# Kernel tuning notes

Hardware: AMD Instinct MI355X
Metric: run time of the kernel (lower is better)

The kernel has to match this reference:

```python
import jax, jax.numpy as jnp
import numpy as np

SL, BS, E, H, PF, STRIDE, SHIFT = 2048, 2, 1024, 16, 16, 1, 0
DH = E // H  # 64


def setup_inputs() -> dict:
    key = jax.random.key(0)
    ks = jax.random.split(key, 6)
    s = 0.02
    return {
        'x': jax.random.normal(ks[0], (SL, BS, E), jnp.float32),
        'ln_g': jnp.ones((E,), jnp.float32),
        'ln_b': jnp.zeros((E,), jnp.float32),
        'Wq': jax.random.normal(ks[1], (E, E), jnp.float32) * s,
        'bq': jnp.zeros((E,), jnp.float32),
        'Wk': jax.random.normal(ks[2], (E, E), jnp.float32) * s,
        'bk': jnp.zeros((E,), jnp.float32),
        'Wv': jax.random.normal(ks[3], (E, E), jnp.float32) * s,
        'bv': jnp.zeros((E,), jnp.float32),
        'Wo': jax.random.normal(ks[4], (E, E), jnp.float32) * s,
        'bo': jnp.zeros((E,), jnp.float32),
    }


def _layernorm(x, g, b, eps=1e-5):
    m = x.mean(-1, keepdims=True)
    v = jnp.var(x, axis=-1, keepdims=True)
    return (x - m) * jax.lax.rsqrt(v + eps) * g + b


def _sparsify(context, h):
    # faithful to sparsify(): r = (arange(h)+1)*stride - pf + shift (+ arange(pf)), mod c
    c = context.shape[0]
    base = (jnp.arange(h) + 1) * STRIDE - PF + SHIFT          # [h]
    idx = (base[None, :] + jnp.arange(PF)[:, None]) % c       # [pf, h]
    return context[idx.reshape(-1)].reshape(PF, h, context.shape[1], context.shape[2])


def reference(x, ln_g, ln_b, Wq, bq, Wk, bk, Wv, bv, Wo, bo):
    sl, bs, e = x.shape
    residual = x
    xn = _layernorm(x, ln_g, ln_b)
    # gather pf-sized local context window per query position (modular wrap)
    fetch = _sparsify(xn, sl)                                  # [pf, sl, bs, E]
    # per-token query (length-1) attending to its pf gathered keys
    q = (xn @ Wq + bq).reshape(sl, bs, H, DH)                  # [sl,bs,H,dh]
    k = (fetch @ Wk + bk).reshape(PF, sl, bs, H, DH)           # [pf,sl,bs,H,dh]
    v = (fetch @ Wv + bv).reshape(PF, sl, bs, H, DH)
    scale = 1.0 / jnp.sqrt(jnp.float32(DH))
    scores = jnp.einsum('sbhd,psbhd->sbhp', q, k) * scale      # [sl,bs,H,pf]
    attn = jax.nn.softmax(scores, axis=-1)
    out = jnp.einsum('sbhp,psbhd->sbhd', attn, v).reshape(sl, bs, e)
    out = out @ Wo + bo                                        # output projection
    # dropout is a no-op in eval
    return residual + out
```

## Files before the change

kernel.cpp:

```cpp
#include <hip/hip_runtime.h>
#include <cstdint>
#include <cstddef>

#define SLEN 2048
#define BSZ  2
#define EDIM 1024
#define NHEAD 16
#define DHEAD 64
#define PFW  16
#define NTOK (SLEN*BSZ)

#define BK 32

typedef __attribute__((ext_vector_type(8))) short short8;
typedef __attribute__((ext_vector_type(4))) float floatx4;

__device__ __forceinline__ short f2bf(float f) {
  union { float f; uint32_t u; } v; v.f = f;
  uint32_t r = v.u + 0x7fffu + ((v.u >> 16) & 1u);
  return (short)(r >> 16);
}
__device__ __forceinline__ float bf2f(short s) {
  union { uint32_t u; float f; } v; v.u = ((uint32_t)(uint16_t)s) << 16;
  return v.f;
}

__device__ __forceinline__ void async16(const void* g, void* l) {
  __builtin_amdgcn_global_load_lds((const __attribute__((address_space(1))) void*)g,
                                   (__attribute__((address_space(3))) void*)l,
                                   16, 0, 0);
}

__global__ __launch_bounds__(256) void prep_kernel(
    const float* __restrict__ x, const float* __restrict__ g,
    const float* __restrict__ b, short* __restrict__ xn,
    const float* __restrict__ W0, const float* __restrict__ W1,
    const float* __restrict__ W2, const float* __restrict__ W3,
    short* __restrict__ Wt_base)
{
  const int bid = blockIdx.x;
  const int tid = threadIdx.x;

  if (bid < NTOK) {
    const int row = bid;
    const float4 v = ((const float4*)(x + (size_t)row * EDIM))[tid];
    float s  = v.x + v.y + v.z + v.w;
    float ss = v.x * v.x + v.y * v.y + v.z * v.z + v.w * v.w;
#pragma unroll
    for (int off = 32; off; off >>= 1) {
      s  += __shfl_xor(s, off);
      ss += __shfl_xor(ss, off);
    }
    __shared__ float ws_s[4], ws_ss[4];
    const int lane = tid & 63, wave = tid >> 6;
    if (lane == 0) { ws_s[wave] = s; ws_ss[wave] = ss; }
    __syncthreads();
    s  = ws_s[0] + ws_s[1] + ws_s[2] + ws_s[3];
    ss = ws_ss[0] + ws_ss[1] + ws_ss[2] + ws_ss[3];

    const float mean = s * (1.0f / EDIM);
    const float var  = ss * (1.0f / EDIM) - mean * mean;
    const float rs   = rsqrtf(var + 1e-5f);

    const float4 gv = ((const float4*)g)[tid];
    const float4 bv = ((const float4*)b)[tid];
    short4 o;
    o.x = f2bf((v.x - mean) * rs * gv.x + bv.x);
    o.y = f2bf((v.y - mean) * rs * gv.y + bv.y);
    o.z = f2bf((v.z - mean) * rs * gv.z + bv.z);
    o.w = f2bf((v.w - mean) * rs * gv.w + bv.w);
    ((short4*)(xn + (size_t)row * EDIM))[tid] = o;
  } else {
    const int t = bid - NTOK;
    const int z = t >> 10;
    const int rem = t & 1023;
    const int n0 = (rem & 31) * 32;
    const int k0 = (rem >> 5) * 32;
    const float* W = (z == 0) ? W0 : (z == 1) ? W1 : (z == 2) ? W2 : W3;
    short* Wt = Wt_base + (size_t)z * EDIM * EDIM;

    __shared__ float tile[32][33];
    const int tx = tid & 31;
    const int ty = tid >> 5;
#pragma unroll
    for (int i = 0; i < 4; ++i)
      tile[ty + i * 8][tx] = W[(size_t)(k0 + ty + i * 8) * EDIM + n0 + tx];
    __syncthreads();
#pragma unroll
    for (int i = 0; i < 4; ++i)
      Wt[(size_t)(n0 + ty + i * 8) * EDIM + k0 + tx] = f2bf(tile[tx][ty + i * 8]);
  }
}

__global__ __launch_bounds__(256) void gemm_qkv(
    const short* __restrict__ xn, const short* __restrict__ Wt_base,
    const float* __restrict__ bq, const float* __restrict__ bk,
    const float* __restrict__ bv, short* __restrict__ qkv_base)
{
  __shared__ short As[128 * BK];
  __shared__ short Bs[128 * BK];

  const int bid  = blockIdx.x;
  const int xcd  = bid & 7;
  const int slot = bid >> 3;
  const int nz   = xcd * 3 + slot / 32;
  const int mt   = slot & 31;
  const int z    = nz >> 3;
  const int nt   = nz & 7;

  const short* Bt   = Wt_base + (size_t)z * EDIM * EDIM;
  const float* bias = (z == 0) ? bq : (z == 1) ? bk : bv;
  short* out        = qkv_base + (size_t)z * NTOK * EDIM;

  const int bm = mt * 128;
  const int bn = nt * 128;
  const int tid  = threadIdx.x;
  const int lane = tid & 63;
  const int wave = tid >> 6;

  floatx4 acc[4][4];
#pragma unroll
  for (int i = 0; i < 4; ++i)
#pragma unroll
    for (int j = 0; j < 4; ++j) { floatx4 zz = {0.f, 0.f, 0.f, 0.f}; acc[i][j] = zz; }

  const int lrow = lane >> 2;
  const int lcol = (lane & 3) * 8;
  const short* gA0 = xn + (size_t)(bm + wave * 32 + lrow) * EDIM + lcol;
  const short* gA1 = gA0 + (size_t)16 * EDIM;
  const short* gB0 = Bt + (size_t)(bn + wave * 32 + lrow) * EDIM + lcol;
  const short* gB1 = gB0 + (size_t)16 * EDIM;
  short* lA0 = As + wave * 1024;
  short* lA1 = lA0 + 512;
  short* lB0 = Bs + wave * 1024;
  short* lB1 = lB0 + 512;

  const int wm = (wave >> 1) * 64;
  const int wn = (wave & 1) * 64;
  const int fr = lane & 15;
  const int fq = (lane >> 4) * 8;

  for (int k0 = 0; k0 < EDIM; k0 += BK) {
    async16(gA0, lA0); async16(gA1, lA1);
    async16(gB0, lB0); async16(gB1, lB1);
    gA0 += BK; gA1 += BK; gB0 += BK; gB1 += BK;
    __syncthreads();

    short8 af[4], bf[4];
#pragma unroll
    for (int mi = 0; mi < 4; ++mi)
      af[mi] = *(const short8*)(As + (size_t)(wm + mi * 16 + fr) * BK + fq);
#pragma unroll
    for (int ni = 0; ni < 4; ++ni)
      bf[ni] = *(const short8*)(Bs + (size_t)(wn + ni * 16 + fr) * BK + fq);
#pragma unroll
    for (int mi = 0; mi < 4; ++mi)
#pragma unroll
      for (int ni = 0; ni < 4; ++ni)
        acc[mi][ni] = __builtin_amdgcn_mfma_f32_16x16x32_bf16(
            af[mi], bf[ni], acc[mi][ni], 0, 0, 0);
    __syncthreads();
  }

  const int r0 = bm + wm + ((lane >> 4) * 4);
  const int c0 = bn + wn + (lane & 15);
#pragma unroll
  for (int mi = 0; mi < 4; ++mi)
#pragma unroll
    for (int ni = 0; ni < 4; ++ni) {
      const floatx4 v = acc[mi][ni];
      const int col = c0 + ni * 16;
      const float bb = bias[col];
#pragma unroll
      for (int r = 0; r < 4; ++r) {
        const int row = r0 + mi * 16 + r;
        out[(size_t)row * EDIM + col] = f2bf(v[r] + bb);
      }
    }
}

__global__ __launch_bounds__(256) void gemm_o(
    const short* __restrict__ Aattn, const short* __restrict__ Wot,
    const float* __restrict__ bo, const float* __restrict__ residual,
    float* __restrict__ out)
{
  __shared__ short As[64 * BK];
  __shared__ short Bs[128 * BK];
  const int bm = blockIdx.x * 64;
  const int bn = blockIdx.y * 128;
  const int tid  = threadIdx.x;
  const int lane = tid & 63;
  const int wave = tid >> 6;

  floatx4 acc[2][4];
#pragma unroll
  for (int i = 0; i < 2; ++i)
#pragma unroll
    for (int j = 0; j < 4; ++j) { floatx4 zz = {0.f, 0.f, 0.f, 0.f}; acc[i][j] = zz; }

  const int lrow = lane >> 2;
  const int lcol = (lane & 3) * 8;
  const short* gA0 = Aattn + (size_t)(bm + wave * 16 + lrow) * EDIM + lcol;
  const short* gB0 = Wot + (size_t)(bn + wave * 32 + lrow) * EDIM + lcol;
  const short* gB1 = gB0 + (size_t)16 * EDIM;
  short* lA0 = As + wave * 512;
  short* lB0 = Bs + wave * 1024;
  short* lB1 = lB0 + 512;

  const int wm = (wave >> 1) * 32;
  const int wn = (wave & 1) * 64;
  const int fr = lane & 15;
  const int fq = (lane >> 4) * 8;

  for (int k0 = 0; k0 < EDIM; k0 += BK) {
    async16(gA0, lA0);
    async16(gB0, lB0); async16(gB1, lB1);
    gA0 += BK; gB0 += BK; gB1 += BK;
    __syncthreads();

    short8 af[2], bf[4];
#pragma unroll
    for (int mi = 0; mi < 2; ++mi)
      af[mi] = *(const short8*)(As + (size_t)(wm + mi * 16 + fr) * BK + fq);
#pragma unroll
    for (int ni = 0; ni < 4; ++ni)
      bf[ni] = *(const short8*)(Bs + (size_t)(wn + ni * 16 + fr) * BK + fq);
#pragma unroll
    for (int mi = 0; mi < 2; ++mi)
#pragma unroll
      for (int ni = 0; ni < 4; ++ni)
        acc[mi][ni] = __builtin_amdgcn_mfma_f32_16x16x32_bf16(
            af[mi], bf[ni], acc[mi][ni], 0, 0, 0);
    __syncthreads();
  }

  const int r0 = bm + wm + ((lane >> 4) * 4);
  const int c0 = bn + wn + (lane & 15);
#pragma unroll
  for (int mi = 0; mi < 2; ++mi)
#pragma unroll
    for (int ni = 0; ni < 4; ++ni) {
      const floatx4 v = acc[mi][ni];
      const int col = c0 + ni * 16;
      const float bb = bo[col];
#pragma unroll
      for (int r = 0; r < 4; ++r) {
        const int row = r0 + mi * 16 + r;
        const size_t idx = (size_t)row * EDIM + col;
        out[idx] = residual[idx] + v[r] + bb;
      }
    }
}

#define VT_LD 80
#define PB_LD 40

__global__ __launch_bounds__(256) void attn_mfma(
    const short* __restrict__ Q, const short* __restrict__ K,
    const short* __restrict__ V, short* __restrict__ O)
{
  const int tid  = threadIdx.x;
  const int lane = tid & 63;
  const int wave = tid >> 6;
  const int quad = lane >> 4;
  const int l16  = lane & 15;

  const int bh = blockIdx.y;
  const int h  = bh & (NHEAD - 1);
  const int b  = bh >> 4;
  const int s_blk = blockIdx.x * 64;
  const int col0  = h * DHEAD;

  __shared__ __align__(16) short VT[64 * VT_LD];
  __shared__ __align__(16) short Pb[4][16 * PB_LD];

  for (int task = tid; task < 320; task += 256) {
    const int kp  = task >> 3;
    const int dg  = task & 7;
    const int kk0 = kp * 2;
    int sA = s_blk - 15 + kk0;
    int sB = sA + 1;
    if (sA < 0) sA += SLEN;  if (sA >= SLEN) sA -= SLEN;
    if (sB < 0) sB += SLEN;  if (sB >= SLEN) sB -= SLEN;
    const short8 vA = *(const short8*)(V + (size_t)(sA * BSZ + b) * EDIM + col0 + dg * 8);
    const short8 vB = *(const short8*)(V + (size_t)(sB * BSZ + b) * EDIM + col0 + dg * 8);
#pragma unroll
    for (int j = 0; j < 8; ++j) {
      const int d = dg * 8 + j;
      const uint32_t pack = (uint32_t)(uint16_t)vA[j] | ((uint32_t)(uint16_t)vB[j] << 16);
      *(uint32_t*)&VT[d * VT_LD + kk0] = pack;
    }
  }

  const int sw = s_blk + wave * 16;
  short8 aq[2];
  {
    const size_t base = (size_t)((sw + l16) * BSZ + b) * EDIM + col0 + quad * 8;
    aq[0] = *(const short8*)(Q + base);
    aq[1] = *(const short8*)(Q + base + 32);
  }
  short8 bkf[2][2];
#pragma unroll
  for (int T = 0; T < 2; ++T) {
    int ks = sw - 15 + T * 16 + l16;
    if (ks < 0) ks += SLEN;
    if (ks >= SLEN) ks -= SLEN;
    const size_t base = (size_t)(ks * BSZ + b) * EDIM + col0 + quad * 8;
    bkf[T][0] = *(const short8*)(K + base);
    bkf[T][1] = *(const short8*)(K + base + 32);
  }

  floatx4 S[2];
  { floatx4 zz = {0.f, 0.f, 0.f, 0.f}; S[0] = zz; S[1] = zz; }
#pragma unroll
  for (int T = 0; T < 2; ++T) {
    S[T] = __builtin_amdgcn_mfma_f32_16x16x32_bf16(aq[0], bkf[T][0], S[T], 0, 0, 0);
    S[T] = __builtin_amdgcn_mfma_f32_16x16x32_bf16(aq[1], bkf[T][1], S[T], 0, 0, 0);
  }

  float sc[2][4];
#pragma unroll
  for (int T = 0; T < 2; ++T)
#pragma unroll
    for (int r = 0; r < 4; ++r) {
      const int m = quad * 4 + r;
      const int c = T * 16 + l16;
      const int d = c - m;
      sc[T][r] = (d >= 0 && d <= 15) ? S[T][r] * 0.125f : -1e30f;
    }
  float mx[4], sm[4];
#pragma unroll
  for (int r = 0; r < 4; ++r) mx[r] = fmaxf(sc[0][r], sc[1][r]);
#pragma unroll
  for (int off = 1; off <= 8; off <<= 1)
#pragma unroll
    for (int r = 0; r < 4; ++r) mx[r] = fmaxf(mx[r], __shfl_xor(mx[r], off));
  float p[2][4];
#pragma unroll
  for (int r = 0; r < 4; ++r) {
    p[0][r] = __expf(sc[0][r] - mx[r]);
    p[1][r] = __expf(sc[1][r] - mx[r]);
    sm[r] = p[0][r] + p[1][r];
  }
#pragma unroll
  for (int off = 1; off <= 8; off <<= 1)
#pragma unroll
    for (int r = 0; r < 4; ++r) sm[r] += __shfl_xor(sm[r], off);

  __syncthreads();

  short* Pw = Pb[wave];
#pragma unroll
  for (int T = 0; T < 2; ++T)
#pragma unroll
    for (int r = 0; r < 4; ++r) {
      const int m = quad * 4 + r;
      const int c = T * 16 + l16;
      Pw[m * PB_LD + c] = f2bf(p[T][r]);
    }
  __syncthreads();
  const short8 ap = *(const short8*)(Pw + l16 * PB_LD + quad * 8);

  floatx4 Oacc[4];
  { floatx4 zz = {0.f, 0.f, 0.f, 0.f}; Oacc[0] = zz; Oacc[1] = zz; Oacc[2] = zz; Oacc[3] = zz; }
#pragma unroll
  for (int nt = 0; nt < 4; ++nt) {
    const short8 bv = *(const short8*)(VT + (nt * 16 + l16) * VT_LD + wave * 16 + quad * 8);
    Oacc[nt] = __builtin_amdgcn_mfma_f32_16x16x32_bf16(ap, bv, Oacc[nt], 0, 0, 0);
  }

#pragma unroll
  for (int nt = 0; nt < 4; ++nt)
#pragma unroll
    for (int r = 0; r < 4; ++r) {
      const int m = quad * 4 + r;
      const size_t idx = (size_t)((sw + m) * BSZ + b) * EDIM + col0 + nt * 16 + l16;
      O[idx] = f2bf(Oacc[nt][r] / sm[r]);
    }
}

extern "C" void kernel_launch(void* const* d_in, const int* in_sizes, int n_in,
                              void* d_out, int out_size, void* d_ws, size_t ws_size,
                              hipStream_t stream) {
  const float* x    = (const float*)d_in[0];
  const float* ln_g = (const float*)d_in[1];
  const float* ln_b = (const float*)d_in[2];
  const float* Wq   = (const float*)d_in[3];
  const float* bq   = (const float*)d_in[4];
  const float* Wk   = (const float*)d_in[5];
  const float* bk   = (const float*)d_in[6];
  const float* Wv   = (const float*)d_in[7];
  const float* bv   = (const float*)d_in[8];
  const float* Wo   = (const float*)d_in[9];
  const float* bo   = (const float*)d_in[10];
  float* out = (float*)d_out;

  char* ws = (char*)d_ws;
  short* xn   = (short*)(ws);
  short* Wt   = (short*)(ws + ((size_t)8  << 20));
  short* QKV  = (short*)(ws + ((size_t)16 << 20));
  short* attn = (short*)(ws + ((size_t)40 << 20));

  prep_kernel<<<NTOK + 4096, 256, 0, stream>>>(x, ln_g, ln_b, xn, Wq, Wk, Wv, Wo, Wt);
  gemm_qkv<<<768, 256, 0, stream>>>(xn, Wt, bq, bk, bv, QKV);
  attn_mfma<<<dim3(SLEN / 64, BSZ * NHEAD), 256, 0, stream>>>(
      QKV, QKV + (size_t)NTOK * EDIM, QKV + (size_t)2 * NTOK * EDIM, attn);
  gemm_o<<<dim3(NTOK / 64, EDIM / 128), 256, 0, stream>>>(
      attn, Wt + (size_t)3 * EDIM * EDIM, bo, x, out);
}
```

Before: 159.4 us.

## Quantize QKV projection to int8 with per-row scales and i8 MFMA

The LayerNorm output is quantized to int8 with a per-token absmax scale, and the transposed Q/K/V weights are quantized to int8 per output row in a new kernel. The QKV GEMM then runs on the i32_16x16x64_i8 MFMA, halving operand bytes and doubling K per instruction, and dequantizes in the epilogue. This trades numerical precision for throughput and adds an extra kernel launch plus a weight requantization pass on every call.

```diff
diff --git a/kernel.cpp b/kernel.cpp
--- a/kernel.cpp
+++ b/kernel.cpp
@@ -14,6 +14,7 @@
 
 typedef __attribute__((ext_vector_type(8))) short short8;
 typedef __attribute__((ext_vector_type(4))) float floatx4;
+typedef __attribute__((ext_vector_type(4))) int   int4v;
 
 __device__ __forceinline__ short f2bf(float f) {
   union { float f; uint32_t u; } v; v.f = f;
@@ -24,6 +25,10 @@
   union { uint32_t u; float f; } v; v.u = ((uint32_t)(uint16_t)s) << 16;
   return v.f;
 }
+__device__ __forceinline__ int q8(float f, float inv) {
+  int q = __float2int_rn(f * inv);
+  return min(127, max(-127, q));
+}
 
 __device__ __forceinline__ void async16(const void* g, void* l) {
   __builtin_amdgcn_global_load_lds((const __attribute__((address_space(1))) void*)g,
@@ -33,7 +38,8 @@
 
 __global__ __launch_bounds__(256) void prep_kernel(
     const float* __restrict__ x, const float* __restrict__ g,
-    const float* __restrict__ b, short* __restrict__ xn,
+    const float* __restrict__ b, char* __restrict__ xn_i8,
+    float* __restrict__ xn_scl,
     const float* __restrict__ W0, const float* __restrict__ W1,
     const float* __restrict__ W2, const float* __restrict__ W3,
     short* __restrict__ Wt_base)
@@ -51,7 +57,7 @@
       s  += __shfl_xor(s, off);
       ss += __shfl_xor(ss, off);
     }
-    __shared__ float ws_s[4], ws_ss[4];
+    __shared__ float ws_s[4], ws_ss[4], ws_m[4];
     const int lane = tid & 63, wave = tid >> 6;
     if (lane == 0) { ws_s[wave] = s; ws_ss[wave] = ss; }
     __syncthreads();
@@ -64,12 +70,24 @@
 
     const float4 gv = ((const float4*)g)[tid];
     const float4 bv = ((const float4*)b)[tid];
-    short4 o;
-    o.x = f2bf((v.x - mean) * rs * gv.x + bv.x);
-    o.y = f2bf((v.y - mean) * rs * gv.y + bv.y);
-    o.z = f2bf((v.z - mean) * rs * gv.z + bv.z);
-    o.w = f2bf((v.w - mean) * rs * gv.w + bv.w);
-    ((short4*)(xn + (size_t)row * EDIM))[tid] = o;
+    const float n0 = (v.x - mean) * rs * gv.x + bv.x;
+    const float n1 = (v.y - mean) * rs * gv.y + bv.y;
+    const float n2 = (v.z - mean) * rs * gv.z + bv.z;
+    const float n3 = (v.w - mean) * rs * gv.w + bv.w;
+
+    float am = fmaxf(fmaxf(fabsf(n0), fabsf(n1)), fmaxf(fabsf(n2), fabsf(n3)));
+#pragma unroll
+    for (int off = 32; off; off >>= 1) am = fmaxf(am, __shfl_xor(am, off));
+    if (lane == 0) ws_m[wave] = am;
+    __syncthreads();
+    am = fmaxf(fmaxf(ws_m[0], ws_m[1]), fmaxf(ws_m[2], ws_m[3]));
+
+    const float inv = (am > 1e-30f) ? 127.0f / am : 0.0f;
+    const int q0 = q8(n0, inv), q1 = q8(n1, inv), q2 = q8(n2, inv), q3 = q8(n3, inv);
+    const uint32_t pack = (uint32_t)(q0 & 0xff) | ((uint32_t)(q1 & 0xff) << 8) |
+                          ((uint32_t)(q2 & 0xff) << 16) | ((uint32_t)(q3 & 0xff) << 24);
+    ((uint32_t*)(xn_i8 + (size_t)row * EDIM))[tid] = pack;
+    if (tid == 0) xn_scl[row] = am * (1.0f / 127.0f);
   } else {
     const int t = bid - NTOK;
     const int z = t >> 10;
@@ -92,13 +110,40 @@
   }
 }
 
-__global__ __launch_bounds__(256) void gemm_qkv(
-    const short* __restrict__ xn, const short* __restrict__ Wt_base,
+__global__ __launch_bounds__(256) void quant_w(
+    const short* __restrict__ Wt, char* __restrict__ w_i8,
+    float* __restrict__ w_scl)
+{
+  const int R = blockIdx.x;
+  const int tid = threadIdx.x;
+  const short4 s4 = ((const short4*)(Wt + (size_t)R * EDIM))[tid];
+  const float w0 = bf2f(s4.x), w1 = bf2f(s4.y), w2 = bf2f(s4.z), w3 = bf2f(s4.w);
+
+  float am = fmaxf(fmaxf(fabsf(w0), fabsf(w1)), fmaxf(fabsf(w2), fabsf(w3)));
+#pragma unroll
+  for (int off = 32; off; off >>= 1) am = fmaxf(am, __shfl_xor(am, off));
+  __shared__ float wm[4];
+  const int lane = tid & 63, wave = tid >> 6;
+  if (lane == 0) wm[wave] = am;
+  __syncthreads();
+  am = fmaxf(fmaxf(wm[0], wm[1]), fmaxf(wm[2], wm[3]));
+
+  const float inv = (am > 1e-30f) ? 127.0f / am : 0.0f;
+  const int q0 = q8(w0, inv), q1 = q8(w1, inv), q2 = q8(w2, inv), q3 = q8(w3, inv);
+  const uint32_t pack = (uint32_t)(q0 & 0xff) | ((uint32_t)(q1 & 0xff) << 8) |
+                        ((uint32_t)(q2 & 0xff) << 16) | ((uint32_t)(q3 & 0xff) << 24);
+  ((uint32_t*)(w_i8 + (size_t)R * EDIM))[tid] = pack;
+  if (tid == 0) w_scl[R] = am * (1.0f / 127.0f);
+}
+
+__global__ __launch_bounds__(256) void gemm_qkv_i8(
+    const char* __restrict__ xn_i8, const float* __restrict__ xn_scl,
+    const char* __restrict__ w_i8, const float* __restrict__ w_scl,
     const float* __restrict__ bq, const float* __restrict__ bk,
     const float* __restrict__ bv, short* __restrict__ qkv_base)
 {
-  __shared__ short As[128 * BK];
-  __shared__ short Bs[128 * BK];
+  __shared__ __align__(16) char As[128 * 64];
+  __shared__ __align__(16) char Bs[128 * 64];
 
   const int bid  = blockIdx.x;
   const int xcd  = bid & 7;
@@ -108,7 +153,8 @@
   const int z    = nz >> 3;
   const int nt   = nz & 7;
 
-  const short* Bt   = Wt_base + (size_t)z * EDIM * EDIM;
+  const char*  Bt   = w_i8 + (size_t)z * EDIM * EDIM;
+  const float* bscl = w_scl + z * EDIM;
   const float* bias = (z == 0) ? bq : (z == 1) ? bk : bv;
   short* out        = qkv_base + (size_t)z * NTOK * EDIM;
 
@@ -118,46 +164,46 @@
   const int lane = tid & 63;
   const int wave = tid >> 6;
 
-  floatx4 acc[4][4];
+  int4v acc[4][4];
 #pragma unroll
   for (int i = 0; i < 4; ++i)
 #pragma unroll
-    for (int j = 0; j < 4; ++j) { floatx4 zz = {0.f, 0.f, 0.f, 0.f}; acc[i][j] = zz; }
-
-  const int lrow = lane >> 2;
-  const int lcol = (lane & 3) * 8;
-  const short* gA0 = xn + (size_t)(bm + wave * 32 + lrow) * EDIM + lcol;
-  const short* gA1 = gA0 + (size_t)16 * EDIM;
-  const short* gB0 = Bt + (size_t)(bn + wave * 32 + lrow) * EDIM + lcol;
-  const short* gB1 = gB0 + (size_t)16 * EDIM;
-  short* lA0 = As + wave * 1024;
-  short* lA1 = lA0 + 512;
-  short* lB0 = Bs + wave * 1024;
-  short* lB1 = lB0 + 512;
-
-  const int wm = (wave >> 1) * 64;
-  const int wn = (wave & 1) * 64;
-  const int fr = lane & 15;
-  const int fq = (lane >> 4) * 8;
-
-  for (int k0 = 0; k0 < EDIM; k0 += BK) {
+    for (int j = 0; j < 4; ++j) { int4v zz = {0, 0, 0, 0}; acc[i][j] = zz; }
+
+  const int lrow  = lane >> 2;
+  const int lcolB = (lane & 3) * 16;
+  const char* gA0 = xn_i8 + (size_t)(bm + wave * 32 + lrow) * EDIM + lcolB;
+  const char* gA1 = gA0 + (size_t)16 * EDIM;
+  const char* gB0 = Bt + (size_t)(bn + wave * 32 + lrow) * EDIM + lcolB;
+  const char* gB1 = gB0 + (size_t)16 * EDIM;
+  char* lA0 = As + wave * 2048;
+  char* lA1 = lA0 + 1024;
+  char* lB0 = Bs + wave * 2048;
+  char* lB1 = lB0 + 1024;
+
+  const int wm  = (wave >> 1) * 64;
+  const int wn  = (wave & 1) * 64;
+  const int fr  = lane & 15;
+  const int fqB = (lane >> 4) * 16;
+
+  for (int k0 = 0; k0 < EDIM; k0 += 64) {
     async16(gA0, lA0); async16(gA1, lA1);
     async16(gB0, lB0); async16(gB1, lB1);
-    gA0 += BK; gA1 += BK; gB0 += BK; gB1 += BK;
-    __syncthreads();
-
-    short8 af[4], bf[4];
+    gA0 += 64; gA1 += 64; gB0 += 64; gB1 += 64;
+    __syncthreads();
+
+    int4v af[4], bf[4];
 #pragma unroll
     for (int mi = 0; mi < 4; ++mi)
-      af[mi] = *(const short8*)(As + (size_t)(wm + mi * 16 + fr) * BK + fq);
+      af[mi] = *(const int4v*)(As + (size_t)(wm + mi * 16 + fr) * 64 + fqB);
 #pragma unroll
     for (int ni = 0; ni < 4; ++ni)
-      bf[ni] = *(const short8*)(Bs + (size_t)(wn + ni * 16 + fr) * BK + fq);
+      bf[ni] = *(const int4v*)(Bs + (size_t)(wn + ni * 16 + fr) * 64 + fqB);
 #pragma unroll
     for (int mi = 0; mi < 4; ++mi)
 #pragma unroll
       for (int ni = 0; ni < 4; ++ni)
-        acc[mi][ni] = __builtin_amdgcn_mfma_f32_16x16x32_bf16(
+        acc[mi][ni] = __builtin_amdgcn_mfma_i32_16x16x64_i8(
             af[mi], bf[ni], acc[mi][ni], 0, 0, 0);
     __syncthreads();
   }
@@ -165,18 +211,23 @@
   const int r0 = bm + wm + ((lane >> 4) * 4);
   const int c0 = bn + wn + (lane & 15);
 #pragma unroll
-  for (int mi = 0; mi < 4; ++mi)
+  for (int mi = 0; mi < 4; ++mi) {
+    float sa[4];
+#pragma unroll
+    for (int r = 0; r < 4; ++r) sa[r] = xn_scl[r0 + mi * 16 + r];
 #pragma unroll
     for (int ni = 0; ni < 4; ++ni) {
-      const floatx4 v = acc[mi][ni];
+      const int4v v = acc[mi][ni];
       const int col = c0 + ni * 16;
+      const float sb = bscl[col];
       const float bb = bias[col];
 #pragma unroll
       for (int r = 0; r < 4; ++r) {
         const int row = r0 + mi * 16 + r;
-        out[(size_t)row * EDIM + col] = f2bf(v[r] + bb);
+        out[(size_t)row * EDIM + col] = f2bf((float)v[r] * (sa[r] * sb) + bb);
       }
     }
+  }
 }
 
 __global__ __launch_bounds__(256) void gemm_o(
@@ -396,13 +447,19 @@
   float* out = (float*)d_out;
 
   char* ws = (char*)d_ws;
-  short* xn   = (short*)(ws);
-  short* Wt   = (short*)(ws + ((size_t)8  << 20));
-  short* QKV  = (short*)(ws + ((size_t)16 << 20));
-  short* attn = (short*)(ws + ((size_t)40 << 20));
-
-  prep_kernel<<<NTOK + 4096, 256, 0, stream>>>(x, ln_g, ln_b, xn, Wq, Wk, Wv, Wo, Wt);
-  gemm_qkv<<<768, 256, 0, stream>>>(xn, Wt, bq, bk, bv, QKV);
+  char*  xn_i8  = ws;
+  short* Wt     = (short*)(ws + ((size_t)4  << 20));
+  char*  w_i8   = ws + ((size_t)12 << 20);
+  short* QKV    = (short*)(ws + ((size_t)15 << 20));
+  short* attn   = (short*)(ws + ((size_t)39 << 20));
+  float* xn_scl = (float*)(ws + ((size_t)47 << 20));
+  float* w_scl  = (float*)(ws + ((size_t)47 << 20) + (1 << 16));
+
+  prep_kernel<<<NTOK + 4096, 256, 0, stream>>>(x, ln_g, ln_b, xn_i8, xn_scl,
+                                               Wq, Wk, Wv, Wo, Wt);
+  quant_w<<<3 * EDIM, 256, 0, stream>>>(Wt, w_i8, w_scl);
+  gemm_qkv_i8<<<768, 256, 0, stream>>>(xn_i8, xn_scl, w_i8, w_scl,
+                                       bq, bk, bv, QKV);
   attn_mfma<<<dim3(SLEN / 64, BSZ * NHEAD), 256, 0, stream>>>(
       QKV, QKV + (size_t)NTOK * EDIM, QKV + (size_t)2 * NTOK * EDIM, attn);
   gemm_o<<<dim3(NTOK / 64, EDIM / 128), 256, 0, stream>>>(
```

Result: faster. 153.3 us (-3.8%).
